# Performance work log

Hardware: AMD Instinct MI355X
Metric: run time of the kernel (lower is better)

The kernel has to match this reference:

```python
import jax, jax.numpy as jnp
import numpy as np

P, E, N = 5, 400000, 50000  # edge types (protocols), edges per type, nodes
NEG_SLOPE = 0.2  # GATv2 leaky_relu default
LAYERS = ["e1", "e2", "e3", "d1", "d2", "d3"]  # encoder 15->8->8->2, decoder 2->8->8->15
DIMS = {"e1": (15, 8), "e2": (8, 8), "e3": (8, 2), "d1": (2, 8), "d2": (8, 8), "d3": (8, 15)}


def setup_inputs() -> dict:
    key = jax.random.key(0)
    ks = iter(jax.random.split(key, 64))

    def p(shape):
        return jax.random.normal(next(ks), shape, dtype=jnp.float32) * 0.1

    inp = {
        "x": jax.random.normal(next(ks), (N, 15), dtype=jnp.float32),
        "edge_attr": jax.random.normal(next(ks), (P, E, 35), dtype=jnp.float32),
        "edge_index": jax.random.randint(next(ks), (P, 2, E), 0, N, dtype=jnp.int32),
    }
    for name, (fi, fo) in DIMS.items():
        inp[f"{name}_wl"] = p((P, fi, fo))
        inp[f"{name}_wr"] = p((P, fi, fo))
        inp[f"{name}_we"] = p((P, 35, fo))
        inp[f"{name}_a"] = p((P, fo))
        inp[f"{name}_b"] = p((P, fo))
    return inp


def _hetero_gatv2(x, edge_index, edge_attr, Wl, Wr, We, att, b):
    """One to_hetero GATv2 layer: per-edge-type GATv2Conv (heads=1, add_self_loops=True,
    fill_value='mean' for self-loop edge_attr), summed over edge types."""
    n = x.shape[0]
    loop = jnp.arange(n, dtype=edge_index.dtype)

    def one(ei, ea, wl, wr, we, a, bb):
        xl = x @ wl  # [N, F] source-side projection
        xr = x @ wr  # [N, F] target-side projection
        s = jnp.concatenate([ei[0], loop])  # add self loops
        d = jnp.concatenate([ei[1], loop])
        # self-loop edge features = mean of edge_attr; project before concat to stay small
        eproj = jnp.concatenate(
            [ea @ we, jnp.broadcast_to(ea.mean(0) @ we, (n, wl.shape[1]))], axis=0
        )  # [E+N, F]
        m = xl[s] + xr[d] + eproj
        e = jax.nn.leaky_relu(m, NEG_SLOPE) @ a  # [E+N] attention logits
        emax = jax.ops.segment_max(e, d, num_segments=n)
        ex = jnp.exp(e - emax[d])
        den = jax.ops.segment_sum(ex, d, num_segments=n)
        alpha = ex / den[d]
        out = jax.ops.segment_sum(alpha[:, None] * xl[s], d, num_segments=n)
        return out + bb

    return jax.vmap(one)(edge_index, edge_attr, Wl, Wr, We, att, b).sum(0)


def _gae(x, edge_index, edge_attr, params):
    h = x
    for name in LAYERS:
        wl, wr, we, a, b = params[name]
        h = _hetero_gatv2(h, edge_index, edge_attr, wl, wr, we, a, b)
        if name not in ("e3", "d3"):  # relu between layers, none after enc/dec output
            h = jax.nn.relu(h)
    return h  # reconstruction [N, 15]


def reference(x, edge_attr, edge_index,
              e1_wl, e1_wr, e1_we, e1_a, e1_b,
              e2_wl, e2_wr, e2_we, e2_a, e2_b,
              e3_wl, e3_wr, e3_we, e3_a, e3_b,
              d1_wl, d1_wr, d1_we, d1_a, d1_b,
              d2_wl, d2_wr, d2_we, d2_a, d2_b,
              d3_wl, d3_wr, d3_we, d3_a, d3_b):
    params = {
        "e1": (e1_wl, e1_wr, e1_we, e1_a, e1_b),
        "e2": (e2_wl, e2_wr, e2_we, e2_a, e2_b),
        "e3": (e3_wl, e3_wr, e3_we, e3_a, e3_b),
        "d1": (d1_wl, d1_wr, d1_we, d1_a, d1_b),
        "d2": (d2_wl, d2_wr, d2_we, d2_a, d2_b),
        "d3": (d3_wl, d3_wr, d3_we, d3_a, d3_b),
    }
    return _gae(x, edge_index, edge_attr, params)
```

## Files before the change

kernel.cpp:

```cpp
#include <hip/hip_runtime.h>
#include <stdint.h>

#define PP 5
#define EE 400000
#define NN 50000
#define PN (PP*NN)
#define EPT (PP*EE)
#define G2 512
#define NGRP (EE/64)
#define NBK ((NN+255)/256)
#define NBKT (PP*NBK)
#define CHUNK 4096
#define NB2 ((EE+CHUNK-1)/CHUNK)

typedef unsigned int u32;
typedef unsigned short u16;
typedef float f32x4 __attribute__((ext_vector_type(4)));
typedef short s16x8 __attribute__((ext_vector_type(8)));
union FAB { s16x8 v; u32 w[4]; };

__device__ __forceinline__ u16 f2bf(float x){
  u32 u = __float_as_uint(x);
  u32 r = (u + 0x7fffu + ((u>>16)&1u))>>16;
  return (u16)r;
}
__device__ __forceinline__ u32 packbf(float a, float b){
  return (u32)f2bf(a) | ((u32)f2bf(b)<<16);
}
__device__ __forceinline__ float bf2f(u32 b){ return __uint_as_float(b<<16); }
__device__ __forceinline__ float lrelu(float x){ return fmaxf(x,0.f)+0.2f*fminf(x,0.f); }

__global__ __launch_bounds__(256) void k_bhist(const int* __restrict__ ei, u32* __restrict__ hist){
  __shared__ u32 sb[NBK];
  const int p=blockIdx.y, blk=blockIdx.x, t=threadIdx.x;
  for(int i=t;i<NBK;i+=256) sb[i]=0u;
  __syncthreads();
  const int* drow = ei + (size_t)(p*2+1)*EE;
  #pragma unroll
  for(int i=0;i<4;i++){
    int e = blk*CHUNK + i*1024 + t*4;
    if(e<EE){
      int4 d4=*(const int4*)&drow[e];
      atomicAdd(&sb[d4.x>>8],1u); atomicAdd(&sb[d4.y>>8],1u);
      atomicAdd(&sb[d4.z>>8],1u); atomicAdd(&sb[d4.w>>8],1u);
    }
  }
  __syncthreads();
  for(int i=t;i<NBK;i+=256) hist[((size_t)(p*NBK+i))*NB2 + blk]=sb[i];
}

__global__ __launch_bounds__(128) void k_bsum(u32* __restrict__ hist, u32* __restrict__ bcnt){
  __shared__ u32 s[128];
  const int g = blockIdx.y*NBK + blockIdx.x;
  const int t = threadIdx.x;
  u32 v = (t<NB2)? hist[(size_t)g*NB2+t] : 0u;
  s[t]=v; __syncthreads();
  for(int o=1;o<128;o<<=1){
    u32 x=(t>=o)?s[t-o]:0u;
    __syncthreads();
    s[t]+=x;
    __syncthreads();
  }
  if(t<NB2) hist[(size_t)g*NB2+t] = s[t]-v;
  if(t==127) bcnt[g]=s[127];
}

__global__ __launch_bounds__(1024) void k_bscan(const u32* __restrict__ bcnt, u32* __restrict__ boff){
  __shared__ u32 s[1024];
  const int t=threadIdx.x;
  u32 v=(t<NBKT)?bcnt[t]:0u;
  s[t]=v; __syncthreads();
  for(int o=1;o<1024;o<<=1){
    u32 x=(t>=o)?s[t-o]:0u;
    __syncthreads();
    s[t]+=x;
    __syncthreads();
  }
  if(t<NBKT) boff[t]=s[t]-v;
  if(t==0) boff[NBKT]=(u32)EPT;
}

__global__ __launch_bounds__(256) void k_bscatter2(const int* __restrict__ ei, const u32* __restrict__ boff,
                                                   const u32* __restrict__ hist, uint2* __restrict__ bedge){
  __shared__ u32 cur[NBK];
  const int p=blockIdx.y, blk=blockIdx.x, t=threadIdx.x;
  if(t<NBK) cur[t] = boff[p*NBK+t] + hist[((size_t)(p*NBK+t))*NB2 + blk];
  __syncthreads();
  const int* srow = ei + (size_t)(p*2  )*EE;
  const int* drow = ei + (size_t)(p*2+1)*EE;
  #pragma unroll
  for(int i=0;i<4;i++){
    int e = blk*CHUNK + i*1024 + t*4;
    if(e<EE){
      int4 s4=*(const int4*)&srow[e];
      int4 d4=*(const int4*)&drow[e];
      u32 p0=atomicAdd(&cur[d4.x>>8],1u);
      u32 p1=atomicAdd(&cur[d4.y>>8],1u);
      u32 p2=atomicAdd(&cur[d4.z>>8],1u);
      u32 p3=atomicAdd(&cur[d4.w>>8],1u);
      bedge[p0]=make_uint2((u32)s4.x|((u32)(d4.x&255)<<16),(u32)(e  ));
      bedge[p1]=make_uint2((u32)s4.y|((u32)(d4.y&255)<<16),(u32)(e+1));
      bedge[p2]=make_uint2((u32)s4.z|((u32)(d4.z&255)<<16),(u32)(e+2));
      bedge[p3]=make_uint2((u32)s4.w|((u32)(d4.w&255)<<16),(u32)(e+3));
    }
  }
}

__global__ __launch_bounds__(256) void k_bfinal2(const uint2* __restrict__ bedge, const u32* __restrict__ boff,
                                                 u32* __restrict__ off, uint2* __restrict__ se){
  __shared__ u32 ncnt[256];
  __shared__ u32 lcur[256];
  const int p=blockIdx.y, b=blockIdx.x, t=threadIdx.x;
  const u32 g=(u32)(p*NBK+b);
  const u32 j0=boff[g], j1=boff[g+1], cnt=j1-j0;
  ncnt[t]=0u; __syncthreads();
  for(u32 i=t;i<cnt;i+=256){
    uint2 v=bedge[j0+i];
    atomicAdd(&ncnt[(v.x>>16)&255u],1u);
  }
  __syncthreads();
  u32 myc=ncnt[t];
  for(int o=1;o<256;o<<=1){
    u32 x=(t>=o)?ncnt[t-o]:0u;
    __syncthreads();
    ncnt[t]+=x;
    __syncthreads();
  }
  const u32 excl=ncnt[t]-myc;
  const int n0=b*256;
  if(n0+t<NN) off[(size_t)p*NN + n0 + t] = j0 + excl;
  if(g==NBKT-1 && t==0) off[PN]=(u32)EPT;
  lcur[t]=j0+excl;
  __syncthreads();
  for(u32 i=t;i<cnt;i+=256){
    uint2 v=bedge[j0+i];
    u32 dl=(v.x>>16)&255u;
    u32 pos=atomicAdd(&lcur[dl],1u);
    se[pos]=make_uint2(v.x&0xffffu, v.y);
  }
}

__global__ __launch_bounds__(256) void k_split(const uint2* __restrict__ se,
                                               u32* __restrict__ srcs, u32* __restrict__ eid){
  size_t i=(size_t)blockIdx.x*256+threadIdx.x;
  if(i<EPT){ uint2 v=se[i]; srcs[i]=v.x; eid[i]=v.y; }
}

__global__ __launch_bounds__(256) void k_eproj_mfma(
    const float* __restrict__ ea, const u32* __restrict__ eid,
    const float* __restrict__ we0, const float* __restrict__ we1,
    const float* __restrict__ we2, const float* __restrict__ we3,
    const float* __restrict__ we4, const float* __restrict__ we5,
    u16* __restrict__ ep0, u16* __restrict__ ep1, u16* __restrict__ ep2,
    u16* __restrict__ ep3, u16* __restrict__ ep4, u16* __restrict__ ep5,
    float* __restrict__ bpartP)
{
  __shared__ u16  sW[64*64];
  __shared__ u16  sEpi[4*16*72];
  __shared__ float sRed[64];

  const int t=threadIdx.x, p=blockIdx.y;
  const int w=t>>6, L=t&63, e16=L&15, quad=L>>4;

  for(int i=t;i<2048;i+=256) ((u32*)sW)[i]=0u;
  if(t<64) sRed[t]=0.f;
  __syncthreads();

  #define FILLW(WPTR,FO,MOFF) { const float* wsrc=(WPTR)+(size_t)p*35*(FO); \
    for(int i=t;i<35*(FO);i+=256){ int k=i/(FO), f=i-k*(FO); \
      sW[((MOFF)+f)*64+k]=f2bf(wsrc[i]); } }
  FILLW(we0,8,0) FILLW(we1,8,8) FILLW(we2,2,16) FILLW(we3,8,24) FILLW(we4,8,32) FILLW(we5,15,48)
  #undef FILLW
  __syncthreads();

  FAB afr[4][2];
  #pragma unroll
  for(int mt=0;mt<4;mt++)
    #pragma unroll
    for(int kf=0;kf<2;kf++)
      afr[mt][kf].v = *(const s16x8*)&sW[(e16+16*mt)*64 + kf*32 + quad*8];

  float sumacc[16];
  #pragma unroll
  for(int i=0;i<16;i++) sumacc[i]=0.f;

  u16* const myEpi = &sEpi[w*1152];

  u32 eedge_next = eid[(size_t)p*EE + (size_t)blockIdx.x*64 + w*16 + e16];

  for(int g=blockIdx.x; g<NGRP; g+=G2){
    const size_t jbase = (size_t)p*EE + (size_t)g*64 + w*16;

    const u32 eedge = eedge_next;
    {
      const int gn = g + G2;
      if(gn < NGRP)
        eedge_next = eid[(size_t)p*EE + (size_t)gn*64 + w*16 + e16];
    }

    const float* row = ea + ((size_t)p*EE + eedge)*35;
    float v0=row[quad*8+0], v1=row[quad*8+1], v2=row[quad*8+2], v3=row[quad*8+3];
    float v4=row[quad*8+4], v5=row[quad*8+5], v6=row[quad*8+6], v7=row[quad*8+7];
    float b0=0.f,b1=0.f,b2=0.f;
    if(quad==0){ b0=row[32]; b1=row[33]; b2=row[34]; }

    FAB fa, fb;
    fa.w[0]=packbf(v0,v1); fa.w[1]=packbf(v2,v3);
    fa.w[2]=packbf(v4,v5); fa.w[3]=packbf(v6,v7);
    fb.w[0]=packbf(b0,b1); fb.w[1]=packbf(b2,0.f);
    fb.w[2]=0u; fb.w[3]=0u;

    f32x4 acc0={0,0,0,0},acc1={0,0,0,0},acc2={0,0,0,0},acc3={0,0,0,0};
    acc0=__builtin_amdgcn_mfma_f32_16x16x32_bf16(afr[0][0].v, fa.v, acc0,0,0,0);
    acc0=__builtin_amdgcn_mfma_f32_16x16x32_bf16(afr[0][1].v, fb.v, acc0,0,0,0);
    acc1=__builtin_amdgcn_mfma_f32_16x16x32_bf16(afr[1][0].v, fa.v, acc1,0,0,0);
    acc1=__builtin_amdgcn_mfma_f32_16x16x32_bf16(afr[1][1].v, fb.v, acc1,0,0,0);
    acc2=__builtin_amdgcn_mfma_f32_16x16x32_bf16(afr[2][0].v, fa.v, acc2,0,0,0);
    acc2=__builtin_amdgcn_mfma_f32_16x16x32_bf16(afr[2][1].v, fb.v, acc2,0,0,0);
    acc3=__builtin_amdgcn_mfma_f32_16x16x32_bf16(afr[3][0].v, fa.v, acc3,0,0,0);
    acc3=__builtin_amdgcn_mfma_f32_16x16x32_bf16(afr[3][1].v, fb.v, acc3,0,0,0);

    #pragma unroll
    for(int r=0;r<4;r++){ sumacc[r]+=acc0[r]; sumacc[4+r]+=acc1[r]; sumacc[8+r]+=acc2[r]; sumacc[12+r]+=acc3[r]; }

    {
      u16* erow=&myEpi[e16*72];
      uint2 q;
      q.x=packbf(acc0[0],acc0[1]); q.y=packbf(acc0[2],acc0[3]);
      *(uint2*)(erow +  0 + 4*quad)=q;
      q.x=packbf(acc1[0],acc1[1]); q.y=packbf(acc1[2],acc1[3]);
      *(uint2*)(erow + 16 + 4*quad)=q;
      q.x=packbf(acc2[0],acc2[1]); q.y=packbf(acc2[2],acc2[3]);
      *(uint2*)(erow + 32 + 4*quad)=q;
      q.x=packbf(acc3[0],acc3[1]); q.y=packbf(acc3[2],acc3[3]);
      *(uint2*)(erow + 48 + 4*quad)=q;
    }
    asm volatile("s_waitcnt lgkmcnt(0)" ::: "memory");

    {
      const int grp=L>>4, e=L&15;
      const u16* erow=&myEpi[e*72];
      if(grp==0)      ((uint4*)ep0)[jbase+e]=*(const uint4*)(erow+ 0);
      else if(grp==1) ((uint4*)ep1)[jbase+e]=*(const uint4*)(erow+ 8);
      else if(grp==2) ((uint4*)ep3)[jbase+e]=*(const uint4*)(erow+24);
      else            ((uint4*)ep4)[jbase+e]=*(const uint4*)(erow+32);
      if(L<32){
        const int e2=L>>1, half=L&1;
        ((uint4*)ep5)[(jbase+e2)*2+half]=*(const uint4*)(&myEpi[e2*72]+48+8*half);
      } else if(L<48){
        const int e2=L-32;
        ((u32*)ep2)[jbase+e2]=*(const u32*)(&myEpi[e2*72]+16);
      }
    }
  }

  #pragma unroll
  for(int i=0;i<16;i++){
    float v=sumacc[i];
    v+=__shfl_xor(v,1); v+=__shfl_xor(v,2); v+=__shfl_xor(v,4); v+=__shfl_xor(v,8);
    sumacc[i]=v;
  }
  if(e16==0){
    #pragma unroll
    for(int mt=0;mt<4;mt++)
      #pragma unroll
      for(int r=0;r<4;r++)
        atomicAdd(&sRed[16*mt+4*quad+r], sumacc[mt*4+r]);
  }
  __syncthreads();
  if(t<64) bpartP[((size_t)p*G2+blockIdx.x)*64+t]=sRed[t];
}

__global__ __launch_bounds__(320) void k_selfvec2(const float* __restrict__ bpartP, float* __restrict__ selfvec){
  int t=threadIdx.x;
  int p=t/64, m=t%64;
  float s=0.f;
  for(int b=0;b<G2;b++) s+=bpartP[((size_t)p*G2+b)*64+m];
  s*=(1.f/EE);
  int l=-1, f=0;
  if(m<8){l=0;f=m;} else if(m<16){l=1;f=m-8;} else if(m<18){l=2;f=m-16;}
  else if(m>=24&&m<32){l=3;f=m-24;} else if(m>=32&&m<40){l=4;f=m-32;}
  else if(m>=48&&m<63){l=5;f=m-48;}
  if(l>=0) selfvec[(size_t)(l*5+p)*16+f]=s;
}

template<int FI,int FO>
__global__ __launch_bounds__(256) void k_proj(
  const float* __restrict__ h, int hs,
  const float* __restrict__ wl, const float* __restrict__ wr,
  float* __restrict__ xl, float* __restrict__ xr)
{
  __shared__ float sl[FI*FO], sr[FI*FO];
  const int t=threadIdx.x, p=blockIdx.y;
  if(t<FI*FO){ sl[t]=wl[(size_t)p*FI*FO+t]; sr[t]=wr[(size_t)p*FI*FO+t]; }
  __syncthreads();
  const int n=blockIdx.x*256+t;
  if(n>=NN) return;
  float hv[FI];
  #pragma unroll
  for(int k=0;k<FI;k++) hv[k]=h[(size_t)n*hs+k];
  const size_t base=((size_t)p*NN+n)*FO;
  #pragma unroll
  for(int f=0;f<FO;f++){
    float al=0.f, ar=0.f;
    #pragma unroll
    for(int k=0;k<FI;k++){ al+=hv[k]*sl[k*FO+f]; ar+=hv[k]*sr[k*FO+f]; }
    xl[base+f]=al; xr[base+f]=ar;
  }
}

template<int FI,int FO,int PO,bool RELU>
__global__ __launch_bounds__(256) void k_comb(
  const float* __restrict__ partial, const float* __restrict__ b,
  const float* __restrict__ wl, const float* __restrict__ wr,
  float* __restrict__ xl, float* __restrict__ xr)
{
  __shared__ float sl[5*FI*FO], sr[5*FI*FO], sbias[FI];
  const int t=threadIdx.x;
  for(int i=t;i<5*FI*FO;i+=256){ sl[i]=wl[i]; sr[i]=wr[i]; }
  if(t<FI){ float s=0.f; for(int p=0;p<PP;p++) s+=b[p*FI+t]; sbias[t]=s; }
  __syncthreads();
  const int n=blockIdx.x*256+t;
  if(n>=NN) return;
  float h[FI];
  #pragma unroll
  for(int f=0;f<FI;f++) h[f]=sbias[f];
  #pragma unroll
  for(int p=0;p<PP;p++){
    const float* src=partial+((size_t)p*NN+n)*FI;
    #pragma unroll
    for(int f=0;f<FI;f++) h[f]+=src[f];
  }
  if(RELU){
    #pragma unroll
    for(int f=0;f<FI;f++) h[f]=fmaxf(h[f],0.f);
  }
  #pragma unroll
  for(int p=0;p<PP;p++){
    const float* wlp=&sl[p*FI*FO];
    const float* wrp=&sr[p*FI*FO];
    const size_t base=((size_t)p*NN+n)*PO;
    #pragma unroll
    for(int f=0;f<FO;f++){
      float al=0.f, ar=0.f;
      #pragma unroll
      for(int k=0;k<FI;k++){ al+=h[k]*wlp[k*FO+f]; ar+=h[k]*wrp[k*FO+f]; }
      xl[base+f]=al; xr[base+f]=ar;
    }
    #pragma unroll
    for(int f=FO;f<PO;f++){ xl[base+f]=0.f; xr[base+f]=0.f; }
  }
}

template<int FO,int PO>
__device__ __forceinline__ void load_row(const float* __restrict__ g, float* arr){
  if constexpr(FO==2){
    float2 v=*(const float2*)g; arr[0]=v.x; arr[1]=v.y;
  } else {
    #pragma unroll
    for(int c=0;c<(FO+3)/4;c++){
      float4 v=((const float4*)g)[c];
      arr[4*c]=v.x;
      if(4*c+1<FO) arr[4*c+1]=v.y;
      if(4*c+2<FO) arr[4*c+2]=v.z;
      if(4*c+3<FO) arr[4*c+3]=v.w;
    }
  }
}

template<int FO,int EPAD,int PO>
__global__ __launch_bounds__(256) void k_agg(
  const float* __restrict__ xl, const float* __restrict__ xr,
  const u32* __restrict__ off, const u32* __restrict__ srcs,
  const u16* __restrict__ ep, const float* __restrict__ avec,
  const float* __restrict__ selfv, float* __restrict__ partial)
{
  const int t=threadIdx.x, p=blockIdx.y;
  const int n=blockIdx.x*64+(t>>2), sub=t&3;
  if(n>=NN) return;
  const int r=p*NN+n;
  float av[FO], xln[FO], xrn[FO];
  #pragma unroll
  for(int f=0;f<FO;f++) av[f]=avec[p*FO+f];
  load_row<FO,PO>(xl+(size_t)r*PO, xln);
  load_row<FO,PO>(xr+(size_t)r*PO, xrn);

  float den=0.f, num[FO];
  #pragma unroll
  for(int f=0;f<FO;f++) num[f]=0.f;
  if(sub==0){
    float e=0.f;
    #pragma unroll
    for(int f=0;f<FO;f++){ float m=xln[f]+xrn[f]+selfv[p*16+f]; e+=lrelu(m)*av[f]; }
    float ex=__expf(e);
    den=ex;
    #pragma unroll
    for(int f=0;f<FO;f++) num[f]=ex*xln[f];
  }
  const u32 j1=off[r+1];
  for(u32 j=off[r]+sub;j<j1;j+=4){
    const u32 s=srcs[j];
    float epv[FO];
    if constexpr(EPAD==8){
      uint4 q=*(const uint4*)(ep+(size_t)j*8);
      epv[0]=bf2f(q.x&0xffffu); epv[1]=bf2f(q.x>>16);
      epv[2]=bf2f(q.y&0xffffu); epv[3]=bf2f(q.y>>16);
      epv[4]=bf2f(q.z&0xffffu); epv[5]=bf2f(q.z>>16);
      epv[6]=bf2f(q.w&0xffffu); epv[7]=bf2f(q.w>>16);
    } else if constexpr(EPAD==2){
      u32 q=*(const u32*)(ep+(size_t)j*2);
      epv[0]=bf2f(q&0xffffu); epv[1]=bf2f(q>>16);
    } else {
      const uint4* qq=(const uint4*)(ep+(size_t)j*16);
      uint4 q0=qq[0], q1=qq[1];
      u32 w[8]={q0.x,q0.y,q0.z,q0.w,q1.x,q1.y,q1.z,q1.w};
      #pragma unroll
      for(int i=0;i<8;i++){
        if(2*i  <FO) epv[2*i  ]=bf2f(w[i]&0xffffu);
        if(2*i+1<FO) epv[2*i+1]=bf2f(w[i]>>16);
      }
    }
    float xls[FO];
    load_row<FO,PO>(xl+((size_t)p*NN+s)*PO, xls);
    float e=0.f;
    #pragma unroll
    for(int f=0;f<FO;f++){ float m=xls[f]+xrn[f]+epv[f]; e+=lrelu(m)*av[f]; }
    const float ex=__expf(e);
    den+=ex;
    #pragma unroll
    for(int f=0;f<FO;f++) num[f]+=ex*xls[f];
  }
  den+=__shfl_xor(den,1); den+=__shfl_xor(den,2);
  #pragma unroll
  for(int f=0;f<FO;f++){ num[f]+=__shfl_xor(num[f],1); num[f]+=__shfl_xor(num[f],2); }
  if(sub==0){
    const float inv=1.f/den;
    float* dst=partial+(size_t)r*PO;
    #pragma unroll
    for(int f=0;f<FO;f++) dst[f]=num[f]*inv;
  }
}

__global__ __launch_bounds__(256) void k_final15(
  const float* __restrict__ partial, const float* __restrict__ b,
  float* __restrict__ out)
{
  __shared__ float sbias[15];
  const int t=threadIdx.x;
  if(t<15){ float s=0.f; for(int p=0;p<PP;p++) s+=b[p*15+t]; sbias[t]=s; }
  __syncthreads();
  const int n=blockIdx.x*256+t;
  if(n>=NN) return;
  float s[15];
  #pragma unroll
  for(int f=0;f<15;f++) s[f]=sbias[f];
  #pragma unroll
  for(int p=0;p<PP;p++){
    const float* src=partial+((size_t)p*NN+n)*16;
    #pragma unroll
    for(int f=0;f<15;f++) s[f]+=src[f];
  }
  #pragma unroll
  for(int f=0;f<15;f++) out[(size_t)n*15+f]=s[f];
}

extern "C" void kernel_launch(void* const* d_in, const int* in_sizes, int n_in,
                              void* d_out, int out_size, void* d_ws, size_t ws_size,
                              hipStream_t stream)
{
  const float* x =(const float*)d_in[0];
  const float* ea=(const float*)d_in[1];
  const int*   ei=(const int*)d_in[2];
  auto W=[&](int l,int k)->const float*{ return (const float*)d_in[3+5*l+k]; };

  char* base=(char*)d_ws; size_t cur=0;
  auto alloc=[&](size_t bytes)->char*{ char* pp=base+cur; cur=(cur+bytes+255)&~(size_t)255; return pp; };
  u32*  off    =(u32*) alloc((size_t)(PN+1)*4);
  u32*  hist   =(u32*) alloc((size_t)NBKT*NB2*4);
  u32*  bcnt   =(u32*) alloc((size_t)NBKT*4);
  u32*  boff   =(u32*) alloc((size_t)(NBKT+1)*4);
  u32*  srcs   =(u32*) alloc((size_t)EPT*4);
  u32*  eid    =(u32*) alloc((size_t)EPT*4);
  float* bpartP=(float*)alloc((size_t)PP*G2*64*4);
  float* selfvec=(float*)alloc(6*PP*16*4);
  float* xl    =(float*)alloc((size_t)PN*16*4);
  float* xr    =(float*)alloc((size_t)PN*16*4);
  float* partial=(float*)alloc((size_t)PN*16*4);
  u16*  ep0    =(u16*) alloc((size_t)EPT*8*2);
  u16*  ep1    =(u16*) alloc((size_t)EPT*8*2);
  u16*  ep2    =(u16*) alloc((size_t)EPT*2*2);
  u16*  ep3    =(u16*) alloc((size_t)EPT*8*2);
  u16*  ep4    =(u16*) alloc((size_t)EPT*8*2);
  u16*  ep5    =(u16*) alloc((size_t)EPT*16*2);
  uint2* bedge =(uint2*)ep5;
  uint2* se    =(uint2*)(ep5 + (size_t)EPT*8);
  (void)ws_size; (void)in_sizes; (void)n_in; (void)out_size;

  dim3 b256(256);
  k_bhist    <<<dim3(NB2,PP),b256,0,stream>>>(ei,hist);
  k_bsum     <<<dim3(NBK,PP),dim3(128),0,stream>>>(hist,bcnt);
  k_bscan    <<<dim3(1),dim3(1024),0,stream>>>(bcnt,boff);
  k_bscatter2<<<dim3(NB2,PP),b256,0,stream>>>(ei,boff,hist,bedge);
  k_bfinal2  <<<dim3(NBK,PP),b256,0,stream>>>(bedge,boff,off,se);
  k_split    <<<dim3((EPT+255)/256),b256,0,stream>>>(se,srcs,eid);
  k_eproj_mfma<<<dim3(G2,PP),b256,0,stream>>>(ea,eid,
              W(0,2),W(1,2),W(2,2),W(3,2),W(4,2),W(5,2),
              ep0,ep1,ep2,ep3,ep4,ep5,bpartP);
  k_selfvec2<<<dim3(1),dim3(320),0,stream>>>(bpartP,selfvec);

  dim3 gproj((NN+255)/256,PP), gagg((NN+63)/64,PP), gnode((NN+255)/256);

  k_proj<15,8><<<gproj,b256,0,stream>>>(x,15,W(0,0),W(0,1),xl,xr);
  k_agg<8,8,8>   <<<gagg ,b256,0,stream>>>(xl,xr,off,srcs,ep0,W(0,3),selfvec+0*80,partial);
  k_comb<8,8,8,true><<<gnode,b256,0,stream>>>(partial,W(0,4),W(1,0),W(1,1),xl,xr);
  k_agg<8,8,8>   <<<gagg ,b256,0,stream>>>(xl,xr,off,srcs,ep1,W(1,3),selfvec+1*80,partial);
  k_comb<8,2,2,true><<<gnode,b256,0,stream>>>(partial,W(1,4),W(2,0),W(2,1),xl,xr);
  k_agg<2,2,2>   <<<gagg ,b256,0,stream>>>(xl,xr,off,srcs,ep2,W(2,3),selfvec+2*80,partial);
  k_comb<2,8,8,false><<<gnode,b256,0,stream>>>(partial,W(2,4),W(3,0),W(3,1),xl,xr);
  k_agg<8,8,8>   <<<gagg ,b256,0,stream>>>(xl,xr,off,srcs,ep3,W(3,3),selfvec+3*80,partial);
  k_comb<8,8,8,true><<<gnode,b256,0,stream>>>(partial,W(3,4),W(4,0),W(4,1),xl,xr);
  k_agg<8,8,8>   <<<gagg ,b256,0,stream>>>(xl,xr,off,srcs,ep4,W(4,3),selfvec+4*80,partial);
  k_comb<8,15,16,true><<<gnode,b256,0,stream>>>(partial,W(4,4),W(5,0),W(5,1),xl,xr);
  k_agg<15,16,16><<<gagg ,b256,0,stream>>>(xl,xr,off,srcs,ep5,W(5,3),selfvec+5*80,partial);
  k_final15<<<gnode,b256,0,stream>>>(partial,W(5,4),(float*)d_out);
}
```

Baseline: 821.1 us.

## Store sources as 16-bit, fuse split into bucket final, parallelize self-vector reduction

The bucket-final kernel now writes 16-bit source indices and edge ids directly, which removes the intermediate packed array and the separate split kernel. The six aggregation kernels read the 16-bit source array, halving index traffic per edge. The self-loop mean reduction moves from one block to 320 wave-sized blocks that each reduce with shuffles, and the eproj grid shrinks from 512 to 408 blocks. Node ids up to 50000 fit in 16 bits, so the narrowing is safe for this problem size.

```diff
diff --git a/kernel.cpp b/kernel.cpp
--- a/kernel.cpp
+++ b/kernel.cpp
@@ -6,7 +6,7 @@
 #define NN 50000
 #define PN (PP*NN)
 #define EPT (PP*EE)
-#define G2 512
+#define G2 408
 #define NGRP (EE/64)
 #define NBK ((NN+255)/256)
 #define NBKT (PP*NBK)
@@ -15,6 +15,7 @@
 
 typedef unsigned int u32;
 typedef unsigned short u16;
+typedef unsigned char u8;
 typedef float f32x4 __attribute__((ext_vector_type(4)));
 typedef short s16x8 __attribute__((ext_vector_type(8)));
 union FAB { s16x8 v; u32 w[4]; };
@@ -107,7 +108,8 @@
 }
 
 __global__ __launch_bounds__(256) void k_bfinal2(const uint2* __restrict__ bedge, const u32* __restrict__ boff,
-                                                 u32* __restrict__ off, uint2* __restrict__ se){
+                                                 u32* __restrict__ off, u16* __restrict__ srcs16,
+                                                 u32* __restrict__ eid){
   __shared__ u32 ncnt[256];
   __shared__ u32 lcur[256];
   const int p=blockIdx.y, b=blockIdx.x, t=threadIdx.x;
@@ -136,14 +138,9 @@
     uint2 v=bedge[j0+i];
     u32 dl=(v.x>>16)&255u;
     u32 pos=atomicAdd(&lcur[dl],1u);
-    se[pos]=make_uint2(v.x&0xffffu, v.y);
-  }
-}
-
-__global__ __launch_bounds__(256) void k_split(const uint2* __restrict__ se,
-                                               u32* __restrict__ srcs, u32* __restrict__ eid){
-  size_t i=(size_t)blockIdx.x*256+threadIdx.x;
-  if(i<EPT){ uint2 v=se[i]; srcs[i]=v.x; eid[i]=v.y; }
+    srcs16[pos]=(u16)(v.x&0xffffu);
+    eid[pos]=v.y;
+  }
 }
 
 __global__ __launch_bounds__(256) void k_eproj_mfma(
@@ -271,17 +268,21 @@
   if(t<64) bpartP[((size_t)p*G2+blockIdx.x)*64+t]=sRed[t];
 }
 
-__global__ __launch_bounds__(320) void k_selfvec2(const float* __restrict__ bpartP, float* __restrict__ selfvec){
-  int t=threadIdx.x;
-  int p=t/64, m=t%64;
+__global__ __launch_bounds__(64) void k_selfvec3(const float* __restrict__ bpartP, float* __restrict__ selfvec){
+  const int b=blockIdx.x;
+  const int p=b>>6, m=b&63, t=threadIdx.x;
   float s=0.f;
-  for(int b=0;b<G2;b++) s+=bpartP[((size_t)p*G2+b)*64+m];
-  s*=(1.f/EE);
-  int l=-1, f=0;
-  if(m<8){l=0;f=m;} else if(m<16){l=1;f=m-8;} else if(m<18){l=2;f=m-16;}
-  else if(m>=24&&m<32){l=3;f=m-24;} else if(m>=32&&m<40){l=4;f=m-32;}
-  else if(m>=48&&m<63){l=5;f=m-48;}
-  if(l>=0) selfvec[(size_t)(l*5+p)*16+f]=s;
+  for(int i=t;i<G2;i+=64) s+=bpartP[((size_t)p*G2+i)*64+m];
+  s+=__shfl_xor(s,1); s+=__shfl_xor(s,2); s+=__shfl_xor(s,4);
+  s+=__shfl_xor(s,8); s+=__shfl_xor(s,16); s+=__shfl_xor(s,32);
+  if(t==0){
+    s*=(1.f/EE);
+    int l=-1, f=0;
+    if(m<8){l=0;f=m;} else if(m<16){l=1;f=m-8;} else if(m<18){l=2;f=m-16;}
+    else if(m>=24&&m<32){l=3;f=m-24;} else if(m>=32&&m<40){l=4;f=m-32;}
+    else if(m>=48&&m<63){l=5;f=m-48;}
+    if(l>=0) selfvec[(size_t)(l*5+p)*16+f]=s;
+  }
 }
 
 template<int FI,int FO>
@@ -371,7 +372,7 @@
 template<int FO,int EPAD,int PO>
 __global__ __launch_bounds__(256) void k_agg(
   const float* __restrict__ xl, const float* __restrict__ xr,
-  const u32* __restrict__ off, const u32* __restrict__ srcs,
+  const u32* __restrict__ off, const u16* __restrict__ srcs16,
   const u16* __restrict__ ep, const float* __restrict__ avec,
   const float* __restrict__ selfv, float* __restrict__ partial)
 {
@@ -399,7 +400,7 @@
   }
   const u32 j1=off[r+1];
   for(u32 j=off[r]+sub;j<j1;j+=4){
-    const u32 s=srcs[j];
+    const u32 s=srcs16[j];
     float epv[FO];
     if constexpr(EPAD==8){
       uint4 q=*(const uint4*)(ep+(size_t)j*8);
@@ -479,7 +480,7 @@
   u32*  hist   =(u32*) alloc((size_t)NBKT*NB2*4);
   u32*  bcnt   =(u32*) alloc((size_t)NBKT*4);
   u32*  boff   =(u32*) alloc((size_t)(NBKT+1)*4);
-  u32*  srcs   =(u32*) alloc((size_t)EPT*4);
+  u16*  srcs16 =(u16*) alloc((size_t)EPT*2);
   u32*  eid    =(u32*) alloc((size_t)EPT*4);
   float* bpartP=(float*)alloc((size_t)PP*G2*64*4);
   float* selfvec=(float*)alloc(6*PP*16*4);
@@ -493,7 +494,6 @@
   u16*  ep4    =(u16*) alloc((size_t)EPT*8*2);
   u16*  ep5    =(u16*) alloc((size_t)EPT*16*2);
   uint2* bedge =(uint2*)ep5;
-  uint2* se    =(uint2*)(ep5 + (size_t)EPT*8);
   (void)ws_size; (void)in_sizes; (void)n_in; (void)out_size;
 
   dim3 b256(256);
@@ -501,26 +501,25 @@
   k_bsum     <<<dim3(NBK,PP),dim3(128),0,stream>>>(hist,bcnt);
   k_bscan    <<<dim3(1),dim3(1024),0,stream>>>(bcnt,boff);
   k_bscatter2<<<dim3(NB2,PP),b256,0,stream>>>(ei,boff,hist,bedge);
-  k_bfinal2  <<<dim3(NBK,PP),b256,0,stream>>>(bedge,boff,off,se);
-  k_split    <<<dim3((EPT+255)/256),b256,0,stream>>>(se,srcs,eid);
+  k_bfinal2  <<<dim3(NBK,PP),b256,0,stream>>>(bedge,boff,off,srcs16,eid);
   k_eproj_mfma<<<dim3(G2,PP),b256,0,stream>>>(ea,eid,
               W(0,2),W(1,2),W(2,2),W(3,2),W(4,2),W(5,2),
               ep0,ep1,ep2,ep3,ep4,ep5,bpartP);
-  k_selfvec2<<<dim3(1),dim3(320),0,stream>>>(bpartP,selfvec);
+  k_selfvec3<<<dim3(PP*64),dim3(64),0,stream>>>(bpartP,selfvec);
 
   dim3 gproj((NN+255)/256,PP), gagg((NN+63)/64,PP), gnode((NN+255)/256);
 
   k_proj<15,8><<<gproj,b256,0,stream>>>(x,15,W(0,0),W(0,1),xl,xr);
-  k_agg<8,8,8>   <<<gagg ,b256,0,stream>>>(xl,xr,off,srcs,ep0,W(0,3),selfvec+0*80,partial);
+  k_agg<8,8,8>   <<<gagg ,b256,0,stream>>>(xl,xr,off,srcs16,ep0,W(0,3),selfvec+0*80,partial);
   k_comb<8,8,8,true><<<gnode,b256,0,stream>>>(partial,W(0,4),W(1,0),W(1,1),xl,xr);
-  k_agg<8,8,8>   <<<gagg ,b256,0,stream>>>(xl,xr,off,srcs,ep1,W(1,3),selfvec+1*80,partial);
+  k_agg<8,8,8>   <<<gagg ,b256,0,stream>>>(xl,xr,off,srcs16,ep1,W(1,3),selfvec+1*80,partial);
   k_comb<8,2,2,true><<<gnode,b256,0,stream>>>(partial,W(1,4),W(2,0),W(2,1),xl,xr);
-  k_agg<2,2,2>   <<<gagg ,b256,0,stream>>>(xl,xr,off,srcs,ep2,W(2,3),selfvec+2*80,partial);
+  k_agg<2,2,2>   <<<gagg ,b256,0,stream>>>(xl,xr,off,srcs16,ep2,W(2,3),selfvec+2*80,partial);
   k_comb<2,8,8,false><<<gnode,b256,0,stream>>>(partial,W(2,4),W(3,0),W(3,1),xl,xr);
-  k_agg<8,8,8>   <<<gagg ,b256,0,stream>>>(xl,xr,off,srcs,ep3,W(3,3),selfvec+3*80,partial);
+  k_agg<8,8,8>   <<<gagg ,b256,0,stream>>>(xl,xr,off,srcs16,ep3,W(3,3),selfvec+3*80,partial);
   k_comb<8,8,8,true><<<gnode,b256,0,stream>>>(partial,W(3,4),W(4,0),W(4,1),xl,xr);
-  k_agg<8,8,8>   <<<gagg ,b256,0,stream>>>(xl,xr,off,srcs,ep4,W(4,3),selfvec+4*80,partial);
+  k_agg<8,8,8>   <<<gagg ,b256,0,stream>>>(xl,xr,off,srcs16,ep4,W(4,3),selfvec+4*80,partial);
   k_comb<8,15,16,true><<<gnode,b256,0,stream>>>(partial,W(4,4),W(5,0),W(5,1),xl,xr);
-  k_agg<15,16,16><<<gagg ,b256,0,stream>>>(xl,xr,off,srcs,ep5,W(5,3),selfvec+5*80,partial);
+  k_agg<15,16,16><<<gagg ,b256,0,stream>>>(xl,xr,off,srcs16,ep5,W(5,3),selfvec+5*80,partial);
   k_final15<<<gnode,b256,0,stream>>>(partial,W(5,4),(float*)d_out);
 }
```

Result: faster. 803.8 us (-2.1%).
